# Kernel tuning notes

Measured on AMD Instinct MI355X. Metric: run time of the kernel, lower is better.

Reference implementation:

```python
import jax, jax.numpy as jnp
import numpy as np

N = 20000      # nodes
E = 320000     # edges (avg degree 16)
G = 256        # graphs
F_NODE = 64
F_EDGE = 16
HID = 256
H, C = 4, 64   # heads, per-head channels
EPS = 1e-5


def setup_inputs() -> dict:
    key = jax.random.key(0)
    ks = jax.random.split(key, 24)
    def rn(k, shape, scale=0.05):
        return jax.random.normal(k, shape, dtype=jnp.float32) * scale
    src = jax.random.randint(ks[0], (E,), 0, N)
    dst = (src + 1 + jax.random.randint(ks[1], (E,), 0, N - 1)) % N  # no pre-existing self loops
    edge_index = jnp.stack([src, dst]).astype(jnp.int32)
    batch = ((jnp.arange(N) * G) // N).astype(jnp.int32)  # contiguous graph ids, all G graphs non-empty
    return {
        'x': rn(ks[2], (N, F_NODE), 1.0),
        'edge_index': edge_index,
        'batch': batch,
        'edge_attr': rn(ks[3], (E, F_EDGE), 1.0),
        'enc_W': rn(ks[4], (F_NODE, HID)),
        'enc_b': jnp.zeros((HID,), jnp.float32),
        'conv_Wl': rn(ks[5], (3, HID, HID)),
        'conv_bl': rn(ks[6], (3, HID)),
        'conv_Wr': rn(ks[7], (3, HID, HID)),
        'conv_br': rn(ks[8], (3, HID)),
        'conv_We': rn(ks[9], (3, F_EDGE, HID)),
        'conv_att': rn(ks[10], (3, H, C)),
        'conv_bias': rn(ks[11], (3, HID)),
        'bn_gamma': jnp.ones((3, HID), jnp.float32),
        'bn_beta': jnp.zeros((3, HID), jnp.float32),
        'bn_mean': rn(ks[12], (3, HID)),
        'bn_var': jax.random.uniform(ks[13], (3, HID), dtype=jnp.float32) + 0.5,
        'cls_W1': rn(ks[14], (2 * HID, HID)),
        'cls_b1': jnp.zeros((HID,), jnp.float32),
        'cls_g1': jnp.ones((HID,), jnp.float32),
        'cls_bt1': jnp.zeros((HID,), jnp.float32),
        'cls_m1': rn(ks[15], (HID,)),
        'cls_v1': jax.random.uniform(ks[16], (HID,), dtype=jnp.float32) + 0.5,
        'cls_W2': rn(ks[17], (HID, HID // 2)),
        'cls_b2': jnp.zeros((HID // 2,), jnp.float32),
        'cls_g2': jnp.ones((HID // 2,), jnp.float32),
        'cls_bt2': jnp.zeros((HID // 2,), jnp.float32),
        'cls_m2': rn(ks[18], (HID // 2,)),
        'cls_v2': jax.random.uniform(ks[19], (HID // 2,), dtype=jnp.float32) + 0.5,
        'cls_W3': rn(ks[20], (HID // 2, 1)),
        'cls_b3': jnp.zeros((1,), jnp.float32),
    }


def _bn(v, g, b, m, var):
    return (v - m) * jax.lax.rsqrt(var + EPS) * g + b


def _gatv2(h, src, dst, eattr, Wl, bl, Wr, br, We, att, bias, n):
    # GATv2Conv (share_weights=False, concat=True) with edge features.
    xl = (h @ Wl + bl).reshape(n, H, C)          # messages come from lin_l(source)
    xr = (h @ Wr + br).reshape(n, H, C)
    ef = (eattr @ We).reshape(-1, H, C)
    z = jax.nn.leaky_relu(xl[src] + xr[dst] + ef, 0.2)   # [E', H, C]
    alpha = jnp.einsum('ehc,hc->eh', z, att)             # [E', H]
    amax = jax.ops.segment_max(alpha, dst, num_segments=n)
    amax = jnp.where(jnp.isfinite(amax), amax, 0.0)
    ex = jnp.exp(alpha - amax[dst])
    den = jax.ops.segment_sum(ex, dst, num_segments=n)
    a = ex / den[dst]                                    # self loops guarantee den > 0
    out = jax.ops.segment_sum(a[:, :, None] * xl[src], dst, num_segments=n)
    return out.reshape(n, H * C) + bias


def reference(x, edge_index, batch, edge_attr, enc_W, enc_b, conv_Wl, conv_bl, conv_Wr, conv_br, conv_We, conv_att, conv_bias, bn_gamma, bn_beta, bn_mean, bn_var, cls_W1, cls_b1, cls_g1, cls_bt1, cls_m1, cls_v1, cls_W2, cls_b2, cls_g2, cls_bt2, cls_m2, cls_v2, cls_W3, cls_b3):
    n = x.shape[0]
    src, dst = edge_index[0], edge_index[1]
    # add self loops with fill_value='mean' (mean of incoming edge_attr per node)
    deg = jax.ops.segment_sum(jnp.ones(src.shape, x.dtype), dst, num_segments=n)
    loop_attr = jax.ops.segment_sum(edge_attr, dst, num_segments=n) / jnp.maximum(deg, 1.0)[:, None]
    loop = jnp.arange(n, dtype=src.dtype)
    src2 = jnp.concatenate([src, loop])
    dst2 = jnp.concatenate([dst, loop])
    ea2 = jnp.concatenate([edge_attr, loop_attr], axis=0)

    h = jax.nn.relu(x @ enc_W + enc_b)
    for i in range(3):  # fixed layer count
        h_in = h
        hc = _gatv2(h, src2, dst2, ea2, conv_Wl[i], conv_bl[i], conv_Wr[i], conv_br[i], conv_We[i], conv_att[i], conv_bias[i], n)
        h = jax.nn.relu(_bn(hc, bn_gamma[i], bn_beta[i], bn_mean[i], bn_var[i])) + h_in

    cnt = jax.ops.segment_sum(jnp.ones((n,), h.dtype), batch, num_segments=G)
    x_mean = jax.ops.segment_sum(h, batch, num_segments=G) / jnp.maximum(cnt, 1.0)[:, None]
    x_max = jax.ops.segment_max(h, batch, num_segments=G)
    xp = jnp.concatenate([x_mean, x_max], axis=1)

    z = jax.nn.relu(_bn(xp @ cls_W1 + cls_b1, cls_g1, cls_bt1, cls_m1, cls_v1))
    z = jax.nn.relu(_bn(z @ cls_W2 + cls_b2, cls_g2, cls_bt2, cls_m2, cls_v2))
    return (z @ cls_W3 + cls_b3)[:, 0]
```

## Files before the change

kernel.cpp:

```cpp
#include <hip/hip_runtime.h>
#include <hip/hip_bf16.h>

#define N_NODES 20000
#define N_EDGES 320000
#define N_E2    (N_EDGES + N_NODES)
#define N_GRAPHS 256
#define HID 256
#define EPS 1e-5f
#define NSCAN 20
#define CPB 4

typedef unsigned short u16;
typedef __attribute__((ext_vector_type(8))) short short8;
typedef __attribute__((ext_vector_type(4))) float f32x4;

__device__ __forceinline__ float b2f(u16 u) {
    union { unsigned int i; float f; } v; v.i = ((unsigned int)u) << 16; return v.f;
}
__device__ __forceinline__ u16 f2b(float f) {
    __hip_bfloat16 h = __float2bfloat16(f);
    return *reinterpret_cast<u16*>(&h);
}

__global__ void k_init(int* cnt, int* cursor) {
    int i = blockIdx.x * 256 + threadIdx.x;
    if (i < N_NODES) { cnt[i] = 1; cursor[i] = 0; }
}

__global__ void k_count(const int* __restrict__ dst, int* __restrict__ cnt) {
    int e = blockIdx.x * 256 + threadIdx.x;
    if (e < N_EDGES) atomicAdd(&cnt[dst[e]], 1);
}

__global__ void k_scan1(const int* __restrict__ cnt, int* __restrict__ rowp, int* __restrict__ part) {
    __shared__ int ls[256];
    int b = blockIdx.x, tid = threadIdx.x;
    int base = b * 1024 + tid * 4;
    int c[4]; int s = 0;
#pragma unroll
    for (int u = 0; u < 4; u++) { int i = base + u; c[u] = (i < N_NODES) ? cnt[i] : 0; s += c[u]; }
    ls[tid] = s; __syncthreads();
    for (int off = 1; off < 256; off <<= 1) {
        int v = (tid >= off) ? ls[tid - off] : 0;
        __syncthreads();
        ls[tid] += v;
        __syncthreads();
    }
    int excl = ls[tid] - s;
#pragma unroll
    for (int u = 0; u < 4; u++) { int i = base + u; if (i < N_NODES) rowp[i] = excl; excl += c[u]; }
    if (tid == 255) part[b] = ls[255];
}

__global__ void k_scan2(int* part, int* rowp) {
    int s = 0;
    for (int b = 0; b < NSCAN; b++) { int v = part[b]; part[b] = s; s += v; }
    rowp[N_NODES] = s;
}

__global__ void k_scan3(int* __restrict__ rowp, const int* __restrict__ part) {
    int b = blockIdx.x, tid = threadIdx.x;
    int add = part[b];
    int base = b * 1024 + tid * 4;
#pragma unroll
    for (int u = 0; u < 4; u++) { int i = base + u; if (i < N_NODES) rowp[i] += add; }
}

__global__ void k_fill(const int* __restrict__ src, const int* __restrict__ dst,
                       const int* __restrict__ rowp, int* __restrict__ cursor,
                       int* __restrict__ csr_src, int* __restrict__ csr_dst,
                       int* __restrict__ csr_aid) {
    int t = blockIdx.x * 256 + threadIdx.x;
    if (t < N_EDGES) {
        int d = dst[t];
        int pos = atomicAdd(&cursor[d], 1);
        int w = rowp[d] + pos;
        csr_src[w] = src[t];
        csr_dst[w] = d;
        csr_aid[w] = t;
    } else if (t < N_E2) {
        int n = t - N_EDGES;
        int pos = atomicAdd(&cursor[n], 1);
        int w = rowp[n] + pos;
        csr_src[w] = n;
        csr_dst[w] = n;
        csr_aid[w] = N_EDGES + n;
    }
}

__global__ void k_pad(int* csr_src, int* csr_dst) {
    int i = threadIdx.x;
    csr_src[N_E2 + i] = 0;
    csr_dst[N_E2 + i] = 0;
}

__global__ void k_loopattr(const int* __restrict__ rowp, const int* __restrict__ csr_aid,
                           const float* __restrict__ edge_attr, float* __restrict__ lattr) {
    int t = blockIdx.x * 256 + threadIdx.x;
    if (t >= N_NODES * 16) return;
    int n = t >> 4, j = t & 15;
    int st = rowp[n], en = rowp[n + 1];
    float s = 0.f;
    for (int i = st; i < en; i++) {
        int aid = csr_aid[i];
        if (aid < N_EDGES) s += edge_attr[(size_t)aid * 16 + j];
    }
    float deg = (float)(en - st - 1);
    lattr[(size_t)n * 16 + j] = s / fmaxf(deg, 1.0f);
}

__global__ void k_eacsr(const int* __restrict__ csr_aid,
                        const float* __restrict__ edge_attr,
                        const float* __restrict__ lattr,
                        u16* __restrict__ ea_bf) {
    int t = blockIdx.x * 256 + threadIdx.x;
    if (t >= N_E2 * 2) return;
    int e = t >> 1, hf = t & 1;
    int aid = csr_aid[e];
    const float* ap = (aid < N_EDGES) ? edge_attr + (size_t)aid * 16
                                      : lattr + (size_t)(aid - N_EDGES) * 16;
    float4 a = ((const float4*)ap)[hf * 2];
    float4 b = ((const float4*)ap)[hf * 2 + 1];
    u16 v[8] = {f2b(a.x), f2b(a.y), f2b(a.z), f2b(a.w),
                f2b(b.x), f2b(b.y), f2b(b.z), f2b(b.w)};
    *(uint4*)(ea_bf + (size_t)t * 8) = *(uint4*)v;
}

__global__ void k_wef(const float* __restrict__ We, u16* __restrict__ Wef) {
    int t = blockIdx.x * 256 + threadIdx.x;
    if (t >= 3 * 16 * 64) return;
    int layer = t >> 10, r = t & 1023;
    int nt = r >> 6, l = r & 63;
    int kc = l >> 4, ch = nt * 16 + (l & 15);
    u16 v[8];
#pragma unroll
    for (int q = 0; q < 8; q++) {
        float x = 0.f;
        if (kc < 2) x = We[(size_t)layer * 4096 + (size_t)(kc * 8 + q) * 256 + ch];
        v[q] = f2b(x);
    }
    *(uint4*)(Wef + (size_t)t * 8) = *(uint4*)v;
}

__global__ void k_xbf(const float* __restrict__ x, u16* __restrict__ xb) {
    int t = blockIdx.x * 256 + threadIdx.x;
    if (t >= N_NODES * 16) return;
    float4 v = ((const float4*)x)[t];
    u16 o[4] = {f2b(v.x), f2b(v.y), f2b(v.z), f2b(v.w)};
    *(ushort4*)(xb + (size_t)t * 4) = *(ushort4*)o;
}

__global__ void k_twg(const float* __restrict__ W, u16* __restrict__ Wt, int K, int N,
                      unsigned int lstride) {
    __shared__ float tile[32][33];
    int layer = blockIdx.z;
    const float* Wp = W + (size_t)layer * K * N;
    u16* Wtp = Wt + (size_t)layer * lstride;
    int bk = blockIdx.x * 32, bn = blockIdx.y * 32;
    int tx = threadIdx.x & 31, ty = threadIdx.x >> 5;
#pragma unroll
    for (int q = 0; q < 4; q++) {
        int k = bk + ty + q * 8;
        tile[ty + q * 8][tx] = Wp[(size_t)k * N + bn + tx];
    }
    __syncthreads();
#pragma unroll
    for (int q = 0; q < 4; q++) {
        int n = bn + ty + q * 8;
        Wtp[(size_t)n * K + bk + tx] = f2b(tile[tx][ty + q * 8]);
    }
}

__global__ void k_blr(const float* __restrict__ bl, const float* __restrict__ br,
                      float* __restrict__ blr) {
    int t = blockIdx.x * 256 + threadIdx.x;
    if (t >= 3 * 512) return;
    int l = t >> 9, c = t & 511;
    blr[t] = (c < 256) ? bl[l * 256 + c] : br[l * 256 + (c - 256)];
}

template <int EPI>
__global__ __launch_bounds__(256) void k_gemm_bf(
    const u16* __restrict__ A, int lda,
    const u16* __restrict__ Bt, int ldb, int K,
    const float* __restrict__ bias,
    u16* __restrict__ Cbf, int ldc, int coff,
    float* __restrict__ Cf, int M)
{
    __shared__ __align__(16) u16 As[128 * 40];
    __shared__ __align__(16) u16 Bs[64 * 40];
    int tid = threadIdx.x;
    int lane = tid & 63, w = tid >> 6;
    int m0 = blockIdx.x * 128, n0 = blockIdx.y * 64;

    f32x4 acc[2][4];
#pragma unroll
    for (int i = 0; i < 2; i++)
#pragma unroll
        for (int j = 0; j < 4; j++) acc[i][j] = (f32x4){0.f, 0.f, 0.f, 0.f};

    int srow = tid >> 2, skc = (tid & 3) * 8;
    int lr = lane & 15, lk = (lane >> 4) * 8;

    int ktiles = K >> 5;
    for (int kt = 0; kt < ktiles; kt++) {
        if (kt) __syncthreads();
#pragma unroll
        for (int q = 0; q < 2; q++) {
            int arow = q * 64 + srow;
            uint4 av = make_uint4(0, 0, 0, 0);
            if (m0 + arow < M)
                av = *(const uint4*)(A + (size_t)(m0 + arow) * lda + kt * 32 + skc);
            *(uint4*)&As[arow * 40 + skc] = av;
        }
        {
            uint4 bv = *(const uint4*)(Bt + (size_t)(n0 + srow) * ldb + kt * 32 + skc);
            *(uint4*)&Bs[srow * 40 + skc] = bv;
        }
        __syncthreads();

        short8 af0 = *(const short8*)&As[(w * 32 + lr) * 40 + lk];
        short8 af1 = *(const short8*)&As[(w * 32 + 16 + lr) * 40 + lk];
        short8 bf[4];
#pragma unroll
        for (int nt = 0; nt < 4; nt++)
            bf[nt] = *(const short8*)&Bs[(nt * 16 + lr) * 40 + lk];
#pragma unroll
        for (int nt = 0; nt < 4; nt++) {
            acc[0][nt] = __builtin_amdgcn_mfma_f32_16x16x32_bf16(af0, bf[nt], acc[0][nt], 0, 0, 0);
            acc[1][nt] = __builtin_amdgcn_mfma_f32_16x16x32_bf16(af1, bf[nt], acc[1][nt], 0, 0, 0);
        }
    }

    int rq = (lane >> 4) * 4;
#pragma unroll
    for (int nt = 0; nt < 4; nt++) {
        int col = n0 + nt * 16 + lr;
        float bv = bias[col];
#pragma unroll
        for (int mt = 0; mt < 2; mt++) {
#pragma unroll
            for (int j = 0; j < 4; j++) {
                int row = m0 + w * 32 + mt * 16 + rq + j;
                if (row < M) {
                    float v = acc[mt][nt][j] + bv;
                    if (EPI == 1) {
                        v = fmaxf(v, 0.f);
                        Cf[(size_t)row * ldc + col] = v;
                        Cbf[(size_t)row * ldc + col] = f2b(v);
                    } else {
                        Cbf[(size_t)row * ldc + coff + col] = f2b(v);
                    }
                }
            }
        }
    }
}

__global__ __launch_bounds__(256) void k_alpha3(
    const u16* __restrict__ xlr,
    const u16* __restrict__ ea_bf,
    const int* __restrict__ csr_src, const int* __restrict__ csr_dst,
    const u16* __restrict__ Wef,
    const float* __restrict__ att,
    float* __restrict__ alpha)
{
    __shared__ __align__(16) u16 wef_s[16 * 64 * 8];
    int tid = threadIdx.x, lane = tid & 63, w = tid >> 6;
    {
        const uint4* s = (const uint4*)Wef;
        uint4* d = (uint4*)wef_s;
#pragma unroll
        for (int q = 0; q < 4; q++) d[q * 256 + tid] = s[q * 256 + tid];
    }
    int eg = lane >> 4, t16 = lane & 15;

    float att_r[16];
#pragma unroll
    for (int q = 0; q < 16; q++) att_r[q] = att[q * 16 + t16];
    __syncthreads();

    for (int it = 0; it < CPB; it++) {
        int chunk = blockIdx.x * CPB + it;
        if (chunk * 64 >= N_E2) break;
        int e_base = chunk * 64 + w * 16;

        short8 afrag = {0, 0, 0, 0, 0, 0, 0, 0};
        if (eg < 2) {
            int e = e_base + t16; if (e > N_E2 - 1) e = N_E2 - 1;
            afrag = *(const short8*)(ea_bf + (size_t)e * 16 + eg * 8);
        }
        int4 s4 = *(const int4*)(csr_src + e_base + eg * 4);
        int4 d4 = *(const int4*)(csr_dst + e_base + eg * 4);
        const u16* xlp[4]; const u16* xrp[4];
        xlp[0] = xlr + (size_t)s4.x * 512;       xlp[1] = xlr + (size_t)s4.y * 512;
        xlp[2] = xlr + (size_t)s4.z * 512;       xlp[3] = xlr + (size_t)s4.w * 512;
        xrp[0] = xlr + (size_t)d4.x * 512 + 256; xrp[1] = xlr + (size_t)d4.y * 512 + 256;
        xrp[2] = xlr + (size_t)d4.z * 512 + 256; xrp[3] = xlr + (size_t)d4.w * 512 + 256;

        float pj[4] = {0.f, 0.f, 0.f, 0.f};
#pragma unroll
        for (int nt = 0; nt < 16; nt++) {
            short8 bfrag = *(const short8*)&wef_s[(nt * 64 + lane) * 8];
            f32x4 D = __builtin_amdgcn_mfma_f32_16x16x32_bf16(
                afrag, bfrag, (f32x4){0.f, 0.f, 0.f, 0.f}, 0, 0, 0);
            int ch = nt * 16 + t16;
#pragma unroll
            for (int j = 0; j < 4; j++) {
                float z = D[j] + b2f(xlp[j][ch]) + b2f(xrp[j][ch]);
                z = fmaxf(z, 0.f) + 0.2f * fminf(z, 0.f);
                pj[j] = fmaf(z, att_r[nt], pj[j]);
            }
            if ((nt & 3) == 3) {
                int hh = nt >> 2;
#pragma unroll
                for (int j = 0; j < 4; j++) {
                    float p = pj[j];
                    p += __shfl_xor(p, 1, 64);
                    p += __shfl_xor(p, 2, 64);
                    p += __shfl_xor(p, 4, 64);
                    p += __shfl_xor(p, 8, 64);
                    int e = e_base + eg * 4 + j;
                    if (t16 == 0 && e < N_E2) alpha[(size_t)e * 4 + hh] = p;
                    pj[j] = 0.f;
                }
            }
        }
    }
}

__global__ __launch_bounds__(256) void k_aggr(
    const u16* __restrict__ xlr, const float* __restrict__ alpha,
    const int* __restrict__ rowp, const int* __restrict__ csr_src,
    const float* __restrict__ cbias,
    const float* __restrict__ bng, const float* __restrict__ bnb,
    const float* __restrict__ bnm, const float* __restrict__ bnv,
    float* __restrict__ h, u16* __restrict__ h_bf)
{
    __shared__ float lex[4][64][4];
    __shared__ int   lsrc[4][64];
    int lane = threadIdx.x & 63;
    int wv = threadIdx.x >> 6;
    int n = blockIdx.x * 4 + wv;
    if (n >= N_NODES) return;
    int st = rowp[n], en = rowp[n + 1];
    int hsel = lane >> 4;
    int c0 = lane * 4;

    float m4[4]  = {-3.0e38f, -3.0e38f, -3.0e38f, -3.0e38f};
    float den4[4] = {0.f, 0.f, 0.f, 0.f};
    float acc[4]  = {0.f, 0.f, 0.f, 0.f};

    for (int cs = st; cs < en; cs += 64) {
        int cnt = min(64, en - cs);
        float a4[4];
        int s_i = 0;
        if (lane < cnt) {
            float4 v = *(const float4*)(alpha + (size_t)(cs + lane) * 4);
            a4[0] = v.x; a4[1] = v.y; a4[2] = v.z; a4[3] = v.w;
            s_i = csr_src[cs + lane];
        } else {
            a4[0] = a4[1] = a4[2] = a4[3] = -3.0e38f;
        }
        float cm[4] = {a4[0], a4[1], a4[2], a4[3]};
#pragma unroll
        for (int o = 32; o >= 1; o >>= 1)
#pragma unroll
            for (int u = 0; u < 4; u++) cm[u] = fmaxf(cm[u], __shfl_xor(cm[u], o, 64));
        float sc[4];
#pragma unroll
        for (int u = 0; u < 4; u++) {
            float nm = fmaxf(m4[u], cm[u]);
            sc[u] = __expf(m4[u] - nm);
            den4[u] *= sc[u];
            m4[u] = nm;
        }
        float scl = sc[hsel];
#pragma unroll
        for (int u = 0; u < 4; u++) acc[u] *= scl;
        float ex[4];
#pragma unroll
        for (int u = 0; u < 4; u++) ex[u] = (lane < cnt) ? __expf(a4[u] - m4[u]) : 0.f;
        float sx[4] = {ex[0], ex[1], ex[2], ex[3]};
#pragma unroll
        for (int o = 32; o >= 1; o >>= 1)
#pragma unroll
            for (int u = 0; u < 4; u++) sx[u] += __shfl_xor(sx[u], o, 64);
#pragma unroll
        for (int u = 0; u < 4; u++) den4[u] += sx[u];
        *(float4*)&lex[wv][lane][0] = make_float4(ex[0], ex[1], ex[2], ex[3]);
        lsrc[wv][lane] = s_i;
        int j = 0;
        for (; j + 8 <= cnt; j += 8) {
            float a[8]; int sj[8];
#pragma unroll
            for (int q = 0; q < 8; q++) { a[q] = lex[wv][j + q][hsel]; sj[q] = lsrc[wv][j + q]; }
            ushort4 xg[8];
#pragma unroll
            for (int q = 0; q < 8; q++) xg[q] = *(const ushort4*)(xlr + (size_t)sj[q] * 512 + c0);
#pragma unroll
            for (int q = 0; q < 8; q++) {
                acc[0] += a[q] * b2f(((const u16*)&xg[q])[0]);
                acc[1] += a[q] * b2f(((const u16*)&xg[q])[1]);
                acc[2] += a[q] * b2f(((const u16*)&xg[q])[2]);
                acc[3] += a[q] * b2f(((const u16*)&xg[q])[3]);
            }
        }
        for (; j < cnt; j++) {
            float a = lex[wv][j][hsel];
            int sj = lsrc[wv][j];
            ushort4 xg = *(const ushort4*)(xlr + (size_t)sj * 512 + c0);
            acc[0] += a * b2f(((const u16*)&xg)[0]);
            acc[1] += a * b2f(((const u16*)&xg)[1]);
            acc[2] += a * b2f(((const u16*)&xg)[2]);
            acc[3] += a * b2f(((const u16*)&xg)[3]);
        }
    }

    float dd = den4[hsel];
    float4 hin = *(const float4*)(h + (size_t)n * 256 + c0);
    float4 cb  = *(const float4*)(cbias + c0);
    float4 gg  = *(const float4*)(bng + c0);
    float4 bb  = *(const float4*)(bnb + c0);
    float4 mm  = *(const float4*)(bnm + c0);
    float4 vv  = *(const float4*)(bnv + c0);
    float hi[4] = {hin.x, hin.y, hin.z, hin.w};
    float cbv[4] = {cb.x, cb.y, cb.z, cb.w};
    float gv[4] = {gg.x, gg.y, gg.z, gg.w};
    float bv[4] = {bb.x, bb.y, bb.z, bb.w};
    float mv[4] = {mm.x, mm.y, mm.z, mm.w};
    float vvv[4] = {vv.x, vv.y, vv.z, vv.w};
    float4 o;
    ushort4 ob;
#pragma unroll
    for (int u = 0; u < 4; u++) {
        float val = acc[u] / dd + cbv[u];
        val = (val - mv[u]) * rsqrtf(vvv[u] + EPS) * gv[u] + bv[u];
        val = fmaxf(val, 0.f) + hi[u];
        ((float*)&o)[u] = val;
        ((u16*)&ob)[u] = f2b(val);
    }
    *(float4*)(h + (size_t)n * 256 + c0) = o;
    *(ushort4*)(h_bf + (size_t)n * 256 + c0) = ob;
}

__global__ __launch_bounds__(256) void k_poolp(
    const float* __restrict__ h, float* __restrict__ psum, float* __restrict__ pmax)
{
    int g = blockIdx.x, p = blockIdx.y, c = threadIdx.x;
    int gst = (g * N_NODES + N_GRAPHS - 1) / N_GRAPHS;
    int gen = ((g + 1) * N_NODES + N_GRAPHS - 1) / N_GRAPHS;
    int len = gen - gst;
    int cst = gst + (len * p) / 8;
    int cen = gst + (len * (p + 1)) / 8;
    float s = 0.f, mx = -3.0e38f;
    for (int i = cst; i < cen; i++) {
        float v = h[(size_t)i * 256 + c];
        s += v;
        mx = fmaxf(mx, v);
    }
    psum[(size_t)(g * 8 + p) * 256 + c] = s;
    pmax[(size_t)(g * 8 + p) * 256 + c] = mx;
}

__global__ __launch_bounds__(256) void k_head(
    const float* __restrict__ psum, const float* __restrict__ pmax,
    const float* __restrict__ W1, const float* __restrict__ b1,
    const float* __restrict__ g1, const float* __restrict__ bt1,
    const float* __restrict__ m1, const float* __restrict__ v1,
    const float* __restrict__ W2, const float* __restrict__ b2,
    const float* __restrict__ g2, const float* __restrict__ bt2,
    const float* __restrict__ m2, const float* __restrict__ v2,
    const float* __restrict__ W3, const float* __restrict__ b3,
    float* __restrict__ out)
{
    __shared__ float xp_s[512];
    __shared__ float z1_s[256];
    __shared__ float z2p[2][128];
    __shared__ float z2_s[128];
    int g = blockIdx.x, c = threadIdx.x;
    int gst = (g * N_NODES + N_GRAPHS - 1) / N_GRAPHS;
    int gen = ((g + 1) * N_NODES + N_GRAPHS - 1) / N_GRAPHS;

    float s = 0.f, mx = -3.0e38f;
#pragma unroll
    for (int p = 0; p < 8; p++) {
        s += psum[(size_t)(g * 8 + p) * 256 + c];
        mx = fmaxf(mx, pmax[(size_t)(g * 8 + p) * 256 + c]);
    }
    xp_s[c] = s / (float)(gen - gst);
    xp_s[256 + c] = mx;
    __syncthreads();

    float a0 = 0.f, a1 = 0.f, a2 = 0.f, a3 = 0.f;
#pragma unroll 4
    for (int k = 0; k < 512; k += 4) {
        a0 = fmaf(xp_s[k + 0], W1[(k + 0) * 256 + c], a0);
        a1 = fmaf(xp_s[k + 1], W1[(k + 1) * 256 + c], a1);
        a2 = fmaf(xp_s[k + 2], W1[(k + 2) * 256 + c], a2);
        a3 = fmaf(xp_s[k + 3], W1[(k + 3) * 256 + c], a3);
    }
    float a = (a0 + a1) + (a2 + a3) + b1[c];
    a = (a - m1[c]) * rsqrtf(v1[c] + EPS) * g1[c] + bt1[c];
    z1_s[c] = fmaxf(a, 0.f);
    __syncthreads();

    {
        int c2 = c & 127, half = c >> 7;
        float b_acc = 0.f;
#pragma unroll 4
        for (int k = 0; k < 128; k++) {
            int kk = half * 128 + k;
            b_acc = fmaf(z1_s[kk], W2[kk * 128 + c2], b_acc);
        }
        z2p[half][c2] = b_acc;
    }
    __syncthreads();
    if (c < 128) {
        float a2v = z2p[0][c] + z2p[1][c] + b2[c];
        a2v = (a2v - m2[c]) * rsqrtf(v2[c] + EPS) * g2[c] + bt2[c];
        z2_s[c] = fmaxf(a2v, 0.f);
    }
    __syncthreads();

    if (c < 64) {
        float a3v = z2_s[c] * W3[c] + z2_s[c + 64] * W3[c + 64];
#pragma unroll
        for (int o = 32; o >= 1; o >>= 1) a3v += __shfl_xor(a3v, o, 64);
        if (c == 0) out[g] = a3v + b3[0];
    }
}

extern "C" void kernel_launch(void* const* d_in, const int* in_sizes, int n_in,
                              void* d_out, int out_size, void* d_ws, size_t ws_size,
                              hipStream_t stream) {
    const float* x         = (const float*)d_in[0];
    const int*   ei        = (const int*)d_in[1];
    const int*   src       = ei;
    const int*   dst       = ei + N_EDGES;
    const float* edge_attr = (const float*)d_in[3];
    const float* enc_W     = (const float*)d_in[4];
    const float* enc_b     = (const float*)d_in[5];
    const float* conv_Wl   = (const float*)d_in[6];
    const float* conv_bl   = (const float*)d_in[7];
    const float* conv_Wr   = (const float*)d_in[8];
    const float* conv_br   = (const float*)d_in[9];
    const float* conv_We   = (const float*)d_in[10];
    const float* conv_att  = (const float*)d_in[11];
    const float* conv_bias = (const float*)d_in[12];
    const float* bn_g      = (const float*)d_in[13];
    const float* bn_b      = (const float*)d_in[14];
    const float* bn_m      = (const float*)d_in[15];
    const float* bn_v      = (const float*)d_in[16];
    const float* cls_W1    = (const float*)d_in[17];
    const float* cls_b1    = (const float*)d_in[18];
    const float* cls_g1    = (const float*)d_in[19];
    const float* cls_bt1   = (const float*)d_in[20];
    const float* cls_m1    = (const float*)d_in[21];
    const float* cls_v1    = (const float*)d_in[22];
    const float* cls_W2    = (const float*)d_in[23];
    const float* cls_b2    = (const float*)d_in[24];
    const float* cls_g2    = (const float*)d_in[25];
    const float* cls_bt2   = (const float*)d_in[26];
    const float* cls_m2    = (const float*)d_in[27];
    const float* cls_v2    = (const float*)d_in[28];
    const float* cls_W3    = (const float*)d_in[29];
    const float* cls_b3    = (const float*)d_in[30];
    float* out = (float*)d_out;

    char* ws = (char*)d_ws;
    size_t off = 0;
    auto alloc = [&](size_t bytes) -> void* {
        void* p = ws + off;
        off += (bytes + 255) & ~(size_t)255;
        return p;
    };
    float* h       = (float*)alloc((size_t)N_NODES * 256 * 4);
    u16*   h_bf    = (u16*)alloc((size_t)N_NODES * 256 * 2);
    u16*   xlr_bf  = (u16*)alloc((size_t)N_NODES * 512 * 2);
    float* lattr   = (float*)alloc((size_t)N_NODES * 16 * 4);
    u16*   ea_bf   = (u16*)alloc((size_t)N_E2 * 16 * 2);
    float* alphas  = (float*)alloc((size_t)N_E2 * 4 * 4);
    u16*   x_bf    = (u16*)alloc((size_t)N_NODES * 64 * 2);
    u16*   enc_Wt  = (u16*)alloc((size_t)64 * 256 * 2);
    u16*   Wtlr    = (u16*)alloc((size_t)3 * 512 * 256 * 2);
    float* blr     = (float*)alloc((size_t)3 * 512 * 4);
    u16*   Wef     = (u16*)alloc((size_t)3 * 16 * 64 * 8 * 2);
    float* psum    = (float*)alloc((size_t)N_GRAPHS * 8 * 256 * 4);
    float* pmax    = (float*)alloc((size_t)N_GRAPHS * 8 * 256 * 4);
    int*   cnt     = (int*)alloc((size_t)N_NODES * 4);
    int*   rowp    = (int*)alloc((size_t)(N_NODES + 1) * 4);
    int*   cursor  = (int*)alloc((size_t)N_NODES * 4);
    int*   csr_src = (int*)alloc((size_t)(N_E2 + 512) * 4);
    int*   csr_dst = (int*)alloc((size_t)(N_E2 + 512) * 4);
    int*   csr_aid = (int*)alloc((size_t)N_E2 * 4);
    int*   part    = (int*)alloc(64 * 4);

    k_init<<<(N_NODES + 255) / 256, 256, 0, stream>>>(cnt, cursor);
    k_count<<<(N_EDGES + 255) / 256, 256, 0, stream>>>(dst, cnt);
    k_scan1<<<NSCAN, 256, 0, stream>>>(cnt, rowp, part);
    k_scan2<<<1, 1, 0, stream>>>(part, rowp);
    k_scan3<<<NSCAN, 256, 0, stream>>>(rowp, part);
    k_fill<<<(N_E2 + 255) / 256, 256, 0, stream>>>(src, dst, rowp, cursor, csr_src, csr_dst, csr_aid);
    k_pad<<<1, 512, 0, stream>>>(csr_src, csr_dst);
    k_loopattr<<<(N_NODES * 16 + 255) / 256, 256, 0, stream>>>(rowp, csr_aid, edge_attr, lattr);
    k_eacsr<<<(N_E2 * 2 + 255) / 256, 256, 0, stream>>>(csr_aid, edge_attr, lattr, ea_bf);

    k_xbf<<<(N_NODES * 16 + 255) / 256, 256, 0, stream>>>(x, x_bf);
    k_twg<<<dim3(2, 8, 1), 256, 0, stream>>>(enc_W, enc_Wt, 64, 256, 64 * 256);
    k_twg<<<dim3(8, 8, 3), 256, 0, stream>>>(conv_Wl, Wtlr, 256, 256, 512 * 256);
    k_twg<<<dim3(8, 8, 3), 256, 0, stream>>>(conv_Wr, Wtlr + 256 * 256, 256, 256, 512 * 256);
    k_blr<<<6, 256, 0, stream>>>(conv_bl, conv_br, blr);
    k_wef<<<12, 256, 0, stream>>>(conv_We, Wef);

    dim3 ggrid((N_NODES + 127) / 128, 4);
    dim3 ggrid2((N_NODES + 127) / 128, 8);
    k_gemm_bf<1><<<ggrid, 256, 0, stream>>>(x_bf, 64, enc_Wt, 64, 64,
                                            enc_b, h_bf, 256, 0, h, N_NODES);

    int nchunks = (N_E2 + 63) / 64;
    int ablocks = (nchunks + CPB - 1) / CPB;
    for (int i = 0; i < 3; i++) {
        k_gemm_bf<0><<<ggrid2, 256, 0, stream>>>(h_bf, 256, Wtlr + (size_t)i * 131072, 256, 256,
                                                 blr + (size_t)i * 512, xlr_bf, 512, 0, nullptr, N_NODES);
        k_alpha3<<<ablocks, 256, 0, stream>>>(
            xlr_bf, ea_bf, csr_src, csr_dst,
            Wef + (size_t)i * 8192, conv_att + (size_t)i * 256, alphas);
        k_aggr<<<N_NODES / 4, 256, 0, stream>>>(
            xlr_bf, alphas, rowp, csr_src,
            conv_bias + (size_t)i * HID,
            bn_g + (size_t)i * HID, bn_b + (size_t)i * HID,
            bn_m + (size_t)i * HID, bn_v + (size_t)i * HID, h, h_bf);
    }

    k_poolp<<<dim3(N_GRAPHS, 8), 256, 0, stream>>>(h, psum, pmax);
    k_head<<<N_GRAPHS, 256, 0, stream>>>(
        psum, pmax, cls_W1, cls_b1, cls_g1, cls_bt1, cls_m1, cls_v1,
        cls_W2, cls_b2, cls_g2, cls_bt2, cls_m2, cls_v2,
        cls_W3, cls_b3, out);
}
```

Baseline: 452.4 us.

## Permute GEMM output layout for vectorized per-edge gathers in alpha kernel

```diff
diff --git a/kernel.cpp b/kernel.cpp
--- a/kernel.cpp
+++ b/kernel.cpp
@@ -184,7 +184,8 @@
     const u16* __restrict__ A, int lda,
     const u16* __restrict__ Bt, int ldb, int K,
     const float* __restrict__ bias,
-    u16* __restrict__ Cbf, int ldc, int coff,
+    u16* __restrict__ Cbf, int ldc,
+    u16* __restrict__ Cp,
     float* __restrict__ Cf, int M)
 {
     __shared__ __align__(16) u16 As[128 * 40];
@@ -249,7 +250,11 @@
                         Cf[(size_t)row * ldc + col] = v;
                         Cbf[(size_t)row * ldc + col] = f2b(v);
                     } else {
-                        Cbf[(size_t)row * ldc + coff + col] = f2b(v);
+                        u16 b = f2b(v);
+                        int half = col >> 8, cc = col & 255;
+                        int p = (half << 8) + ((cc & 15) << 4) + (cc >> 4);
+                        Cp[(size_t)row * 512 + p] = b;
+                        if (half == 0) Cbf[(size_t)row * 256 + col] = b;
                     }
                 }
             }
@@ -258,7 +263,7 @@
 }
 
 __global__ __launch_bounds__(256) void k_alpha3(
-    const u16* __restrict__ xlr,
+    const u16* __restrict__ xlr_p,
     const u16* __restrict__ ea_bf,
     const int* __restrict__ csr_src, const int* __restrict__ csr_dst,
     const u16* __restrict__ Wef,
@@ -292,11 +297,20 @@
         }
         int4 s4 = *(const int4*)(csr_src + e_base + eg * 4);
         int4 d4 = *(const int4*)(csr_dst + e_base + eg * 4);
-        const u16* xlp[4]; const u16* xrp[4];
-        xlp[0] = xlr + (size_t)s4.x * 512;       xlp[1] = xlr + (size_t)s4.y * 512;
-        xlp[2] = xlr + (size_t)s4.z * 512;       xlp[3] = xlr + (size_t)s4.w * 512;
-        xrp[0] = xlr + (size_t)d4.x * 512 + 256; xrp[1] = xlr + (size_t)d4.y * 512 + 256;
-        xrp[2] = xlr + (size_t)d4.z * 512 + 256; xrp[3] = xlr + (size_t)d4.w * 512 + 256;
+        int sj[4] = {s4.x, s4.y, s4.z, s4.w};
+        int dj[4] = {d4.x, d4.y, d4.z, d4.w};
+
+        uint4 xlv[4][2], xrv[4][2];
+#pragma unroll
+        for (int j = 0; j < 4; j++) {
+            const u16* bp = xlr_p + (size_t)sj[j] * 512 + t16 * 16;
+            xlv[j][0] = *(const uint4*)(bp);
+            xlv[j][1] = *(const uint4*)(bp + 8);
+            const u16* bq = xlr_p + (size_t)dj[j] * 512 + 256 + t16 * 16;
+            xrv[j][0] = *(const uint4*)(bq);
+            xrv[j][1] = *(const uint4*)(bq + 8);
+        }
+        __builtin_amdgcn_sched_barrier(0);
 
         float pj[4] = {0.f, 0.f, 0.f, 0.f};
 #pragma unroll
@@ -304,10 +318,11 @@
             short8 bfrag = *(const short8*)&wef_s[(nt * 64 + lane) * 8];
             f32x4 D = __builtin_amdgcn_mfma_f32_16x16x32_bf16(
                 afrag, bfrag, (f32x4){0.f, 0.f, 0.f, 0.f}, 0, 0, 0);
-            int ch = nt * 16 + t16;
 #pragma unroll
             for (int j = 0; j < 4; j++) {
-                float z = D[j] + b2f(xlp[j][ch]) + b2f(xrp[j][ch]);
+                u16 xl = ((const u16*)&xlv[j][nt >> 3])[nt & 7];
+                u16 xr = ((const u16*)&xrv[j][nt >> 3])[nt & 7];
+                float z = D[j] + b2f(xl) + b2f(xr);
                 z = fmaxf(z, 0.f) + 0.2f * fminf(z, 0.f);
                 pj[j] = fmaf(z, att_r[nt], pj[j]);
             }
@@ -330,7 +345,8 @@
 }
 
 __global__ __launch_bounds__(256) void k_aggr(
-    const u16* __restrict__ xlr, const float* __restrict__ alpha,
+    const u16* __restrict__ xl_bf,
+    const float* __restrict__ alpha,
     const int* __restrict__ rowp, const int* __restrict__ csr_src,
     const float* __restrict__ cbias,
     const float* __restrict__ bng, const float* __restrict__ bnb,
@@ -397,7 +413,7 @@
             for (int q = 0; q < 8; q++) { a[q] = lex[wv][j + q][hsel]; sj[q] = lsrc[wv][j + q]; }
             ushort4 xg[8];
 #pragma unroll
-            for (int q = 0; q < 8; q++) xg[q] = *(const ushort4*)(xlr + (size_t)sj[q] * 512 + c0);
+            for (int q = 0; q < 8; q++) xg[q] = *(const ushort4*)(xl_bf + (size_t)sj[q] * 256 + c0);
 #pragma unroll
             for (int q = 0; q < 8; q++) {
                 acc[0] += a[q] * b2f(((const u16*)&xg[q])[0]);
@@ -409,7 +425,7 @@
         for (; j < cnt; j++) {
             float a = lex[wv][j][hsel];
             int sj = lsrc[wv][j];
-            ushort4 xg = *(const ushort4*)(xlr + (size_t)sj * 512 + c0);
+            ushort4 xg = *(const ushort4*)(xl_bf + (size_t)sj * 256 + c0);
             acc[0] += a * b2f(((const u16*)&xg)[0]);
             acc[1] += a * b2f(((const u16*)&xg)[1]);
             acc[2] += a * b2f(((const u16*)&xg)[2]);
@@ -577,7 +593,8 @@
     };
     float* h       = (float*)alloc((size_t)N_NODES * 256 * 4);
     u16*   h_bf    = (u16*)alloc((size_t)N_NODES * 256 * 2);
-    u16*   xlr_bf  = (u16*)alloc((size_t)N_NODES * 512 * 2);
+    u16*   xl_bf   = (u16*)alloc((size_t)N_NODES * 256 * 2);
+    u16*   xlr_p   = (u16*)alloc((size_t)N_NODES * 512 * 2);
     float* lattr   = (float*)alloc((size_t)N_NODES * 16 * 4);
     u16*   ea_bf   = (u16*)alloc((size_t)N_E2 * 16 * 2);
     float* alphas  = (float*)alloc((size_t)N_E2 * 4 * 4);
@@ -616,18 +633,18 @@
     dim3 ggrid((N_NODES + 127) / 128, 4);
     dim3 ggrid2((N_NODES + 127) / 128, 8);
     k_gemm_bf<1><<<ggrid, 256, 0, stream>>>(x_bf, 64, enc_Wt, 64, 64,
-                                            enc_b, h_bf, 256, 0, h, N_NODES);
+                                            enc_b, h_bf, 256, nullptr, h, N_NODES);
 
     int nchunks = (N_E2 + 63) / 64;
     int ablocks = (nchunks + CPB - 1) / CPB;
     for (int i = 0; i < 3; i++) {
         k_gemm_bf<0><<<ggrid2, 256, 0, stream>>>(h_bf, 256, Wtlr + (size_t)i * 131072, 256, 256,
-                                                 blr + (size_t)i * 512, xlr_bf, 512, 0, nullptr, N_NODES);
+                                                 blr + (size_t)i * 512, xl_bf, 512, xlr_p, nullptr, N_NODES);
         k_alpha3<<<ablocks, 256, 0, stream>>>(
-            xlr_bf, ea_bf, csr_src, csr_dst,
+            xlr_p, ea_bf, csr_src, csr_dst,
             Wef + (size_t)i * 8192, conv_att + (size_t)i * 256, alphas);
         k_aggr<<<N_NODES / 4, 256, 0, stream>>>(
-            xlr_bf, alphas, rowp, csr_src,
+            xl_bf, alphas, rowp, csr_src,
             conv_bias + (size_t)i * HID,
             bn_g + (size_t)i * HID, bn_b + (size_t)i * HID,
             bn_m + (size_t)i * HID, bn_v + (size_t)i * HID, h, h_bf);
```

Result: slower. 610.2 us (+34.9%).

## Fuse CSR preprocessing kernels and halve attention chunks per block

Applied to the files above, without the earlier changes.

```diff
diff --git a/kernel.cpp b/kernel.cpp
--- a/kernel.cpp
+++ b/kernel.cpp
@@ -8,7 +8,7 @@
 #define HID 256
 #define EPS 1e-5f
 #define NSCAN 20
-#define CPB 4
+#define CPB 2
 
 typedef unsigned short u16;
 typedef __attribute__((ext_vector_type(8))) short short8;
@@ -20,11 +20,6 @@
 __device__ __forceinline__ u16 f2b(float f) {
     __hip_bfloat16 h = __float2bfloat16(f);
     return *reinterpret_cast<u16*>(&h);
-}
-
-__global__ void k_init(int* cnt, int* cursor) {
-    int i = blockIdx.x * 256 + threadIdx.x;
-    if (i < N_NODES) { cnt[i] = 1; cursor[i] = 0; }
 }
 
 __global__ void k_count(const int* __restrict__ dst, int* __restrict__ cnt) {
@@ -38,7 +33,7 @@
     int base = b * 1024 + tid * 4;
     int c[4]; int s = 0;
 #pragma unroll
-    for (int u = 0; u < 4; u++) { int i = base + u; c[u] = (i < N_NODES) ? cnt[i] : 0; s += c[u]; }
+    for (int u = 0; u < 4; u++) { int i = base + u; c[u] = (i < N_NODES) ? cnt[i] + 1 : 0; s += c[u]; }
     ls[tid] = s; __syncthreads();
     for (int off = 1; off < 256; off <<= 1) {
         int v = (tid >= off) ? ls[tid - off] : 0;
@@ -85,45 +80,46 @@
         csr_src[w] = n;
         csr_dst[w] = n;
         csr_aid[w] = N_EDGES + n;
-    }
-}
-
-__global__ void k_pad(int* csr_src, int* csr_dst) {
-    int i = threadIdx.x;
-    csr_src[N_E2 + i] = 0;
-    csr_dst[N_E2 + i] = 0;
-}
-
-__global__ void k_loopattr(const int* __restrict__ rowp, const int* __restrict__ csr_aid,
-                           const float* __restrict__ edge_attr, float* __restrict__ lattr) {
-    int t = blockIdx.x * 256 + threadIdx.x;
-    if (t >= N_NODES * 16) return;
-    int n = t >> 4, j = t & 15;
-    int st = rowp[n], en = rowp[n + 1];
-    float s = 0.f;
-    for (int i = st; i < en; i++) {
-        int aid = csr_aid[i];
-        if (aid < N_EDGES) s += edge_attr[(size_t)aid * 16 + j];
-    }
-    float deg = (float)(en - st - 1);
-    lattr[(size_t)n * 16 + j] = s / fmaxf(deg, 1.0f);
-}
-
-__global__ void k_eacsr(const int* __restrict__ csr_aid,
+    } else if (t < N_E2 + 512) {
+        csr_src[t] = 0;
+        csr_dst[t] = 0;
+    }
+}
+
+__global__ void k_eacsr(const int* __restrict__ csr_aid, const int* __restrict__ rowp,
                         const float* __restrict__ edge_attr,
-                        const float* __restrict__ lattr,
                         u16* __restrict__ ea_bf) {
     int t = blockIdx.x * 256 + threadIdx.x;
     if (t >= N_E2 * 2) return;
     int e = t >> 1, hf = t & 1;
     int aid = csr_aid[e];
-    const float* ap = (aid < N_EDGES) ? edge_attr + (size_t)aid * 16
-                                      : lattr + (size_t)(aid - N_EDGES) * 16;
-    float4 a = ((const float4*)ap)[hf * 2];
-    float4 b = ((const float4*)ap)[hf * 2 + 1];
-    u16 v[8] = {f2b(a.x), f2b(a.y), f2b(a.z), f2b(a.w),
-                f2b(b.x), f2b(b.y), f2b(b.z), f2b(b.w)};
-    *(uint4*)(ea_bf + (size_t)t * 8) = *(uint4*)v;
+    float v[8];
+    if (aid < N_EDGES) {
+        const float4* ap = (const float4*)(edge_attr + (size_t)aid * 16 + hf * 8);
+        float4 a = ap[0], b = ap[1];
+        v[0] = a.x; v[1] = a.y; v[2] = a.z; v[3] = a.w;
+        v[4] = b.x; v[5] = b.y; v[6] = b.z; v[7] = b.w;
+    } else {
+        int n = aid - N_EDGES;
+        int st = rowp[n], en = rowp[n + 1];
+        float s[8] = {0.f, 0.f, 0.f, 0.f, 0.f, 0.f, 0.f, 0.f};
+        for (int i = st; i < en; i++) {
+            int a2 = csr_aid[i];
+            if (a2 < N_EDGES) {
+                const float4* ap = (const float4*)(edge_attr + (size_t)a2 * 16 + hf * 8);
+                float4 a = ap[0], b = ap[1];
+                s[0] += a.x; s[1] += a.y; s[2] += a.z; s[3] += a.w;
+                s[4] += b.x; s[5] += b.y; s[6] += b.z; s[7] += b.w;
+            }
+        }
+        float rdeg = 1.0f / fmaxf((float)(en - st - 1), 1.0f);
+#pragma unroll
+        for (int q = 0; q < 8; q++) v[q] = s[q] * rdeg;
+    }
+    u16 o[8];
+#pragma unroll
+    for (int q = 0; q < 8; q++) o[q] = f2b(v[q]);
+    *(uint4*)(ea_bf + (size_t)t * 8) = *(uint4*)o;
 }
 
 __global__ void k_wef(const float* __restrict__ We, u16* __restrict__ Wef) {
@@ -578,7 +574,6 @@
     float* h       = (float*)alloc((size_t)N_NODES * 256 * 4);
     u16*   h_bf    = (u16*)alloc((size_t)N_NODES * 256 * 2);
     u16*   xlr_bf  = (u16*)alloc((size_t)N_NODES * 512 * 2);
-    float* lattr   = (float*)alloc((size_t)N_NODES * 16 * 4);
     u16*   ea_bf   = (u16*)alloc((size_t)N_E2 * 16 * 2);
     float* alphas  = (float*)alloc((size_t)N_E2 * 4 * 4);
     u16*   x_bf    = (u16*)alloc((size_t)N_NODES * 64 * 2);
@@ -588,23 +583,23 @@
     u16*   Wef     = (u16*)alloc((size_t)3 * 16 * 64 * 8 * 2);
     float* psum    = (float*)alloc((size_t)N_GRAPHS * 8 * 256 * 4);
     float* pmax    = (float*)alloc((size_t)N_GRAPHS * 8 * 256 * 4);
-    int*   cnt     = (int*)alloc((size_t)N_NODES * 4);
+    int*   cntcur  = (int*)alloc((size_t)2 * N_NODES * 4);
+    int*   cnt     = cntcur;
+    int*   cursor  = cntcur + N_NODES;
     int*   rowp    = (int*)alloc((size_t)(N_NODES + 1) * 4);
-    int*   cursor  = (int*)alloc((size_t)N_NODES * 4);
     int*   csr_src = (int*)alloc((size_t)(N_E2 + 512) * 4);
     int*   csr_dst = (int*)alloc((size_t)(N_E2 + 512) * 4);
     int*   csr_aid = (int*)alloc((size_t)N_E2 * 4);
     int*   part    = (int*)alloc(64 * 4);
 
-    k_init<<<(N_NODES + 255) / 256, 256, 0, stream>>>(cnt, cursor);
+    hipMemsetAsync(cntcur, 0, (size_t)2 * N_NODES * 4, stream);
     k_count<<<(N_EDGES + 255) / 256, 256, 0, stream>>>(dst, cnt);
     k_scan1<<<NSCAN, 256, 0, stream>>>(cnt, rowp, part);
     k_scan2<<<1, 1, 0, stream>>>(part, rowp);
     k_scan3<<<NSCAN, 256, 0, stream>>>(rowp, part);
-    k_fill<<<(N_E2 + 255) / 256, 256, 0, stream>>>(src, dst, rowp, cursor, csr_src, csr_dst, csr_aid);
-    k_pad<<<1, 512, 0, stream>>>(csr_src, csr_dst);
-    k_loopattr<<<(N_NODES * 16 + 255) / 256, 256, 0, stream>>>(rowp, csr_aid, edge_attr, lattr);
-    k_eacsr<<<(N_E2 * 2 + 255) / 256, 256, 0, stream>>>(csr_aid, edge_attr, lattr, ea_bf);
+    k_fill<<<(N_E2 + 512 + 255) / 256, 256, 0, stream>>>(src, dst, rowp, cursor,
+                                                         csr_src, csr_dst, csr_aid);
+    k_eacsr<<<(N_E2 * 2 + 255) / 256, 256, 0, stream>>>(csr_aid, rowp, edge_attr, ea_bf);
 
     k_xbf<<<(N_NODES * 16 + 255) / 256, 256, 0, stream>>>(x, x_bf);
     k_twg<<<dim3(2, 8, 1), 256, 0, stream>>>(enc_W, enc_Wt, 64, 256, 64 * 256);
```

Result: faster. 432.7 us (median of 3 runs) (-4.3%).
